# Performance work log

Hardware: AMD Instinct MI355X
Metric: run time of the kernel (lower is better)

Reference implementation:

```python
import jax, jax.numpy as jnp
import numpy as np
import math

TEMP = 30.0          # softmax temperature in RelationUnit
EPS_L2 = 1e-12       # F.normalize eps
EPS_IN = 1e-5        # InstanceL2Norm eps

def _l2n(x):
    n = jnp.sqrt(jnp.sum(x * x, axis=-1, keepdims=True))
    return x / jnp.maximum(n, EPS_L2)

def com_attn(qr, qi, kr, ki, vr, vi, Wk, bk):
    # seq layout [L, B, D]; complex QK^T with shared WK projection, per-branch softmax
    pr = _l2n(qr @ Wk + bk); pi = _l2n(qi @ Wk + bk)
    sr = _l2n(kr @ Wk + bk); si = _l2n(ki @ Wk + bk)
    dr = jnp.einsum('qbd,kbd->bqk', pr, sr) - jnp.einsum('qbd,kbd->bqk', pi, si)
    di = jnp.einsum('qbd,kbd->bqk', pr, si) + jnp.einsum('qbd,kbd->bqk', pi, sr)
    Ar = jax.nn.softmax(dr * TEMP, axis=-1)
    Ai = jax.nn.softmax(di * TEMP, axis=-1)
    outr = jnp.einsum('bqk,kbd->qbd', Ar, vr) - jnp.einsum('bqk,kbd->qbd', Ai, vi)
    outi = jnp.einsum('bqk,kbd->qbd', Ar, vi) + jnp.einsum('bqk,kbd->qbd', Ai, vr)
    return outr, outi

def inorm(src, n, b, d, h, w, scale):
    # src: [n*h*w, b, d] -> per-(img,batch) L2 instance norm over (d,h,w)
    x = src.reshape(n, h, w, b, d).transpose(0, 3, 4, 1, 2).reshape(n * b, d, h, w)
    cnt = float(d * h * w)
    ss = jnp.sum(x * x, axis=(1, 2, 3), keepdims=True)
    x = x * (scale * jnp.sqrt(cnt / (ss + EPS_IN)))
    return x.reshape(n, b, d, h * w).transpose(0, 3, 1, 2).reshape(n * h * w, b, d)

def to_seq(x):
    n, b, d, h, w = x.shape
    return x.reshape(n, b, d, h * w).transpose(0, 3, 1, 2).reshape(n * h * w, b, d)

def setup_inputs() -> dict:
    key = jax.random.key(0)
    ks = jax.random.split(key, 10)
    NT, NS, B, D, H, W, KD = 3, 3, 8, 512, 22, 22, 128
    f = jnp.float32
    return {
        'train_feat': jax.random.normal(ks[0], (NT, B, D, H, W), f),
        'test_feat': jax.random.normal(ks[1], (NS, B, D, H, W), f),
        'train_label': jax.random.uniform(ks[2], (NT, B, H, W), f),
        'Wk_en': jax.random.normal(ks[3], (D, D), f) * 0.02,
        'bk_en': jax.random.normal(ks[4], (D,), f) * 0.02,
        'Wk_self': jax.random.normal(ks[5], (D, KD), f) * 0.02,
        'bk_self': jax.random.normal(ks[6], (KD,), f) * 0.02,
        'Wk_cross': jax.random.normal(ks[7], (D, KD), f) * 0.02,
        'bk_cross': jax.random.normal(ks[8], (KD,), f) * 0.02,
        'Wc': jax.random.normal(ks[9], (D, 2 * D), f) * 0.02,
    }

def reference(train_feat, test_feat, train_label, Wk_en, bk_en, Wk_self, bk_self, Wk_cross, bk_cross, Wc):
    nt, b, d, h, w = train_feat.shape
    ns = test_feat.shape[0]
    scale = math.sqrt(1.0 / (d * 4 * 4))
    # ---- encoder (imag branch starts at zero) ----
    sr = to_seq(train_feat)
    si = jnp.zeros_like(sr)
    ar, ai = com_attn(sr, si, sr, si, sr, si, Wk_en, bk_en)
    mem_r = inorm(sr + ar, nt, b, d, h, w, scale)
    mem_i = inorm(si + ai, nt, b, d, h, w, scale)
    # ---- positional (label) map broadcast to feature dim ----
    pr = train_label.reshape(nt, b, 1, h * w).transpose(0, 3, 1, 2).reshape(nt * h * w, b, 1)
    pr = jnp.broadcast_to(pr, (nt * h * w, b, d))
    pi = jnp.zeros_like(pr)
    # ---- single decoder layer, applied per image (memory/pos shared) ----
    def dec(tr, ti):
        inl = lambda s: inorm(s, 1, b, d, h, w, scale)
        s2r, s2i = com_attn(tr, ti, tr, ti, tr, ti, Wk_self, bk_self)
        t1r = inl(tr + s2r); t1i = inl(ti + s2i)
        mkr, mki = com_attn(t1r, t1i, mem_r, mem_i, pr, pi, Wk_cross, bk_cross)
        t2r = inl(t1r * mkr); t2i = inl(t1i * mki)
        c3r, c3i = com_attn(t1r, t1i, mem_r, mem_i, mem_r * pr, mem_i * pi, Wk_cross, bk_cross)
        t4r = inl(t1r + c3r); t4i = inl(t1i + c3i)
        outr = inl(t2r + t4r); outi = inl(t2i + t4i)
        fr = outr.reshape(h, w, b, d).transpose(2, 3, 0, 1)  # [b,d,h,w]
        fi = outi.reshape(h, w, b, d).transpose(2, 3, 0, 1)
        return fr, fi
    def per_img_seq(x):  # [n,b,d,h,w] -> [n, h*w, b, d]
        n = x.shape[0]
        return x.reshape(n, b, d, h * w).transpose(0, 3, 1, 2)
    tr_seq = per_img_seq(train_feat)
    enc_r, enc_i = jax.vmap(dec)(tr_seq, jnp.zeros_like(tr_seq))  # [nt,b,d,h,w]
    te_seq = per_img_seq(test_feat)
    dec_r, dec_i = jax.vmap(dec)(te_seq, jnp.zeros_like(te_seq))  # [ns,b,d,h,w]
    # ---- 1x1 compress conv on cat([real, imag], channel) ----
    enc_feat = jnp.einsum('nbchw,oc->nbohw', jnp.concatenate([enc_r, enc_i], axis=2), Wc).reshape(nt * b, d, h, w)
    dec_feat = jnp.einsum('nbchw,oc->nbohw', jnp.concatenate([dec_r, dec_i], axis=2), Wc).reshape(ns * b, d, h, w)
    return jnp.concatenate([enc_feat, dec_feat], axis=0)
```

## Files before the change

kernel.cpp:

```cpp
#include <hip/hip_runtime.h>


namespace {

constexpr int kNI = 3;
constexpr int kB  = 8;
constexpr int kD  = 512;
constexpr int kKD = 128;
constexpr int kHW = 484;
constexpr int kL  = kNI * kHW;
constexpr int kLp = 1456;
constexpr int kHWp = 488;
constexpr float kTemp = 30.0f;
constexpr float kCnt  = 247808.0f;
constexpr float kScaleN = 0.011048543456039806f;
constexpr int kR = kHW * kB;
constexpr int kR6 = 6 * kR;

#define CDIV(a, b) (((a) + (b) - 1) / (b))

typedef float f32x4 __attribute__((ext_vector_type(4)));
typedef unsigned int u32x4 __attribute__((ext_vector_type(4)));
typedef unsigned short u16b;

__device__ __forceinline__ float wsum(float v) {
#pragma unroll
  for (int o = 32; o; o >>= 1) v += __shfl_down(v, o);
  return v;
}
__device__ __forceinline__ float wmax(float v) {
#pragma unroll
  for (int o = 32; o; o >>= 1) v = fmaxf(v, __shfl_down(v, o));
  return v;
}

__device__ __forceinline__ unsigned pk2bf(float lo, float hi) {
  union { float f; unsigned u; } a, b;
  a.f = lo; b.f = hi;
  unsigned ra = (a.u + 0x7FFFu + ((a.u >> 16) & 1u)) >> 16;
  unsigned rb = (b.u + 0x7FFFu + ((b.u >> 16) & 1u)) >> 16;
  return (ra & 0xFFFFu) | (rb << 16);
}
__device__ __forceinline__ u16b f2bf(float x) {
  union { float f; unsigned u; } a;
  a.f = x;
  return (u16b)((a.u + 0x7FFFu + ((a.u >> 16) & 1u)) >> 16);
}
__device__ __forceinline__ float bf2f(u16b x) {
  union { unsigned u; float f; } a;
  a.u = (unsigned)x << 16;
  return a.f;
}

__device__ __forceinline__ void mfma_bf16(f32x4& d, const u32x4& a, const u32x4& b) {
  asm("v_mfma_f32_16x16x32_bf16 %0, %1, %2, %0" : "+v"(d) : "v"(a), "v"(b));
}

__device__ __forceinline__ void ldsbar() {
  asm volatile("s_waitcnt lgkmcnt(0)" ::: "memory");
  __builtin_amdgcn_s_barrier();
  asm volatile("" ::: "memory");
}

__global__ void k_toseq(const float* __restrict__ in, float* __restrict__ out) {
  __shared__ float tile[32][33];
  int nb = blockIdx.z;
  int n = nb / kB, b = nb % kB;
  int p0 = blockIdx.x * 32, d0 = blockIdx.y * 32;
  int tx = threadIdx.x, ty = threadIdx.y;
#pragma unroll
  for (int j = 0; j < 4; ++j) {
    int d = d0 + ty + j * 8, p = p0 + tx;
    if (d < kD && p < kHW) tile[ty + j * 8][tx] = in[(long)nb * kD * kHW + (long)d * kHW + p];
  }
  __syncthreads();
#pragma unroll
  for (int j = 0; j < 4; ++j) {
    int p = p0 + ty + j * 8, d = d0 + tx;
    if (p < kHW && d < kD)
      out[((long)(n * kHW + p) * kB + b) * kD + d] = tile[tx][ty + j * 8];
  }
}

__global__ void k_cvt2d(const float* __restrict__ in, u16b* __restrict__ out, int C, int Cp) {
  long r = blockIdx.x;
  for (int c = threadIdx.x; c < C; c += 256)
    out[r * Cp + c] = f2bf(in[r * (long)C + c]);
}

__global__ void k_tcvt(const float* __restrict__ in, u16b* __restrict__ out, int R, int C) {
  __shared__ float tile[32][33];
  int c0 = blockIdx.x * 32, r0 = blockIdx.y * 32;
  int tx = threadIdx.x, ty = threadIdx.y;
#pragma unroll
  for (int j = 0; j < 4; ++j) {
    int r = r0 + ty + j * 8, c = c0 + tx;
    if (r < R && c < C) tile[ty + j * 8][tx] = in[(long)r * C + c];
  }
  __syncthreads();
#pragma unroll
  for (int j = 0; j < 4; ++j) {
    int c = c0 + ty + j * 8, r = r0 + tx;
    if (r < R && c < C) out[(long)c * R + r] = f2bf(tile[tx][ty + j * 8]);
  }
}

__global__ void k_vrt(const float* __restrict__ mr, const float* __restrict__ lab,
                      u16b* __restrict__ vt) {
  __shared__ float tile[32][33];
  int l0 = blockIdx.x * 32, d0 = blockIdx.y * 32, b = blockIdx.z;
  int tx = threadIdx.x, ty = threadIdx.y;
#pragma unroll
  for (int j = 0; j < 4; ++j) {
    int l = l0 + ty + j * 8;
    if (l < kL)
      tile[ty + j * 8][tx] = mr[((long)l * kB + b) * kD + d0 + tx] * lab[(long)l * kB + b];
  }
  __syncthreads();
#pragma unroll
  for (int j = 0; j < 4; ++j) {
    int d = d0 + ty + j * 8, l = l0 + tx;
    if (l < kL) vt[((long)b * kD + d) * kLp + l] = f2bf(tile[tx][ty + j * 8]);
  }
}

__global__ void k_lab(const float* __restrict__ tl, float* __restrict__ lab) {
  long i = (long)blockIdx.x * 256 + threadIdx.x;
  const long tot = (long)kNI * kB * kHW;
  if (i >= tot) return;
  int p = (int)(i % kHW);
  long t = i / kHW;
  int b = (int)(t % kB);
  int n = (int)(t / kB);
  lab[(long)(n * kHW + p) * kB + b] = tl[i];
}

__global__ void k_l2n_vec(const float* __restrict__ src, float* __restrict__ u, int C) {
  __shared__ float red[2];
  int tid = threadIdx.x;
  float s = 0.f;
  for (int c = tid; c < C; c += 128) { float x = src[c]; s += x * x; }
  s = wsum(s);
  if ((tid & 63) == 0) red[tid >> 6] = s;
  __syncthreads();
  float inv = 1.f / fmaxf(sqrtf(red[0] + red[1]), 1e-12f);
  for (int c = tid; c < C; c += 128) u[c] = src[c] * inv;
}

template <int BM, int BN, bool AF32, bool ACC>
__global__ __launch_bounds__(256) void k_gemm(const void* Ap, const u16b* __restrict__ B,
                                              float* __restrict__ C, int M, int N, int K,
                                              int lda, int ldb, int ldc,
                                              long sA1, long sA2, long sB1, long sB2,
                                              long sC1, long sC2,
                                              const float* __restrict__ addv) {
  const int gx = gridDim.x, gy = gridDim.y;
  const int nwg = gx * gy * gridDim.z;
  const int orig = (blockIdx.z * gy + blockIdx.y) * gx + blockIdx.x;
  const int q = nwg >> 3, rr = nwg & 7, xcd = orig & 7, idx = orig >> 3;
  const int swz = (xcd < rr ? xcd * (q + 1) : rr * (q + 1) + (xcd - rr) * q) + idx;
  const int bx = swz % gx;
  const int tmp = swz / gx;
  const int by = tmp % gy, bz = tmp / gy;
  const int za = bz >> 3, zb = bz & 7;

  const char* Ab = (const char*)Ap + (za * sA1 + zb * sA2) * (AF32 ? 4 : 2);
  const u16b* Bb = B + za * sB1 + zb * sB2;
  C += za * sC1 + zb * sC2;
  constexpr int FM = BM / 32, FN = BN / 32;
  constexpr int NSA = BM * 8 / 256;
  constexpr int NSB = BN * 8 / 256;
  const int m0 = by * BM, n0 = bx * BN;
  const int tid = threadIdx.x;
  const int wid = tid >> 6, lane = tid & 63;
  const int wr = wid >> 1, wc = wid & 1;
  const int fr = lane & 15, fk = lane >> 4;

  __shared__ unsigned AsU[BM * 36];
  __shared__ unsigned BsU[BN * 36];
  f32x4 acc[FM][FN] = {};

  u32x4 pa[NSA];
  float4 paf[AF32 ? 2 * NSA : 1];
  u32x4 pb[NSB];

  auto loadA = [&](int k0) {
#pragma unroll
    for (int i = 0; i < NSA; ++i) {
      int si = tid + i * 256;
      int row = si >> 3, c = si & 7;
      int gr = m0 + row, gk = k0 + c * 8;
      if constexpr (AF32) {
        const float* A = (const float*)Ab;
        if (gr < M && gk + 8 <= K) {
          const float* ap = A + (long)gr * lda + gk;
          paf[2 * i] = *(const float4*)ap;
          paf[2 * i + 1] = *(const float4*)(ap + 4);
        } else {
          float v[8];
#pragma unroll
          for (int j = 0; j < 8; ++j)
            v[j] = (gr < M && gk + j < K) ? A[(long)gr * lda + gk + j] : 0.f;
          paf[2 * i] = make_float4(v[0], v[1], v[2], v[3]);
          paf[2 * i + 1] = make_float4(v[4], v[5], v[6], v[7]);
        }
      } else {
        const u16b* A = (const u16b*)Ab;
        if (gr < M && gk + 8 <= K) {
          pa[i] = *(const u32x4*)(A + (long)gr * lda + gk);
        } else {
          unsigned v[8];
#pragma unroll
          for (int j = 0; j < 8; ++j)
            v[j] = (gr < M && gk + j < K) ? A[(long)gr * lda + gk + j] : 0u;
          pa[i].x = v[0] | (v[1] << 16); pa[i].y = v[2] | (v[3] << 16);
          pa[i].z = v[4] | (v[5] << 16); pa[i].w = v[6] | (v[7] << 16);
        }
      }
    }
  };
  auto loadB = [&](int k0) {
#pragma unroll
    for (int i = 0; i < NSB; ++i) {
      int si = tid + i * 256;
      int row = si >> 3, c = si & 7;
      int gr = n0 + row, gk = k0 + c * 8;
      if (gr < N && gk + 8 <= K) {
        pb[i] = *(const u32x4*)(Bb + (long)gr * ldb + gk);
      } else {
        unsigned v[8];
#pragma unroll
        for (int j = 0; j < 8; ++j)
          v[j] = (gr < N && gk + j < K) ? Bb[(long)gr * ldb + gk + j] : 0u;
        pb[i].x = v[0] | (v[1] << 16); pb[i].y = v[2] | (v[3] << 16);
        pb[i].z = v[4] | (v[5] << 16); pb[i].w = v[6] | (v[7] << 16);
      }
    }
  };
  auto storeAB = [&]() {
#pragma unroll
    for (int i = 0; i < NSA; ++i) {
      int si = tid + i * 256;
      int row = si >> 3, c = si & 7;
      u32x4 w;
      if constexpr (AF32) {
        float4 u0 = paf[2 * i], u1 = paf[2 * i + 1];
        w.x = pk2bf(u0.x, u0.y); w.y = pk2bf(u0.z, u0.w);
        w.z = pk2bf(u1.x, u1.y); w.w = pk2bf(u1.z, u1.w);
      } else {
        w = pa[i];
      }
      *(u32x4*)&AsU[row * 36 + c * 4] = w;
    }
#pragma unroll
    for (int i = 0; i < NSB; ++i) {
      int si = tid + i * 256;
      int row = si >> 3, c = si & 7;
      *(u32x4*)&BsU[row * 36 + c * 4] = pb[i];
    }
  };

  loadA(0);
  loadB(0);
  storeAB();
  __syncthreads();
  const int nk = CDIV(K, 64);
  for (int t = 0; t < nk; ++t) {
    const bool more = (t + 1 < nk);
    if (more) { loadA((t + 1) * 64); loadB((t + 1) * 64); }
#pragma unroll
    for (int kk = 0; kk < 2; ++kk) {
      u32x4 af[FM], bf[FN];
#pragma unroll
      for (int mi = 0; mi < FM; ++mi)
        af[mi] = *(const u32x4*)&AsU[(wr * (BM / 2) + mi * 16 + fr) * 36 + kk * 16 + fk * 4];
#pragma unroll
      for (int ni = 0; ni < FN; ++ni)
        bf[ni] = *(const u32x4*)&BsU[(wc * (BN / 2) + ni * 16 + fr) * 36 + kk * 16 + fk * 4];
#pragma unroll
      for (int mi = 0; mi < FM; ++mi)
#pragma unroll
        for (int ni = 0; ni < FN; ++ni) mfma_bf16(acc[mi][ni], af[mi], bf[ni]);
    }
    if (more) {
      __syncthreads();
      storeAB();
      __syncthreads();
    }
  }
  asm volatile("s_nop 7\n\ts_nop 7" ::: );
#pragma unroll
  for (int mi = 0; mi < FM; ++mi) {
#pragma unroll
    for (int r = 0; r < 4; ++r) {
      int gm = m0 + wr * (BM / 2) + mi * 16 + fk * 4 + r;
      if (gm >= M) continue;
      float av = addv ? addv[(long)za * (kD * 8) + (long)gm * 8 + zb] : 0.f;
#pragma unroll
      for (int ni = 0; ni < FN; ++ni) {
        int gn = n0 + wc * (BN / 2) + ni * 16 + fr;
        if (gn >= N) continue;
        long idx2 = (long)gm * ldc + gn;
        float v = acc[mi][ni][r] + av;
        C[idx2] = ACC ? (C[idx2] + v) : v;
      }
    }
  }
}

template <bool LAB, bool KIMG, bool VZ>
__global__ __launch_bounds__(256) void k_flash(const u16b* __restrict__ Q,
                                               const u16b* __restrict__ K,
                                               const u16b* __restrict__ V,
                                               const float* __restrict__ labv,
                                               u16b* __restrict__ O,
                                               float* __restrict__ mkout,
                                               int S, int ldv) {
  int orig = blockIdx.x;
  int b = orig & 7;
  int t = orig >> 3;
  int qt0 = (t & 15) * 32;
  int img = t >> 4;
  int z = img * 8 + b;
  int tid = threadIdx.x, wid = tid >> 6, lane = tid & 63;
  int fr = lane & 15, fk = lane >> 4;

  __shared__ float Ssm[32 * 68];
  __shared__ unsigned Plds[32 * 36];
  __shared__ float mrun[32], lrun[32], scal[32], mka[32];

  const long qbase = ((long)img * kR + b) * kKD;
  const long kbase = KIMG ? ((long)img * kR + b) * kKD : (long)b * kKD;
  const long vbase = (long)(VZ ? z : b) * kD * ldv;

  u32x4 afq[2][4];
#pragma unroll
  for (int mi = 0; mi < 2; ++mi) {
    int qq = qt0 + mi * 16 + fr;
    if (qq >= kHW) qq = kHW - 1;
#pragma unroll
    for (int kk = 0; kk < 4; ++kk)
      afq[mi][kk] = *(const u32x4*)(Q + qbase + (long)qq * (kB * kKD) + kk * 32 + fk * 8);
  }

  f32x4 oacc[2][8] = {};
  if (tid < 32) { mrun[tid] = -3.0e38f; lrun[tid] = 0.f; mka[tid] = 0.f; }
  __syncthreads();

  int r8 = lane >> 3, i8 = lane & 7;
  int srow = wid * 8 + r8;

  u32x4 kcur[4], knxt[4];
  {
    int krow = wid * 16 + fr;
    int kc = krow < S ? krow : S - 1;
    const u16b* kp = K + kbase + (long)kc * (kB * kKD);
#pragma unroll
    for (int kk = 0; kk < 4; ++kk) kcur[kk] = *(const u32x4*)(kp + kk * 32 + fk * 8);
  }

  for (int kt = 0; kt < S; kt += 64) {
    f32x4 sacc[2] = {};
#pragma unroll
    for (int kk = 0; kk < 4; ++kk) {
      mfma_bf16(sacc[0], afq[0][kk], kcur[kk]);
      mfma_bf16(sacc[1], afq[1][kk], kcur[kk]);
    }
    u32x4 vreg[2][8];
#pragma unroll
    for (int kk = 0; kk < 2; ++kk) {
      int kidx = kt + kk * 32 + fk * 8;
      if (kidx > ldv - 8) kidx = ldv - 8;
#pragma unroll
      for (int n = 0; n < 8; ++n) {
        int d = wid * 128 + n * 16 + fr;
        vreg[kk][n] = *(const u32x4*)(V + vbase + (long)d * ldv + kidx);
      }
    }
    const bool more = (kt + 64 < S);
    if (more) {
      int krow2 = kt + 64 + wid * 16 + fr;
      int kc2 = krow2 < S ? krow2 : S - 1;
      const u16b* kp2 = K + kbase + (long)kc2 * (kB * kKD);
#pragma unroll
      for (int kk = 0; kk < 4; ++kk) knxt[kk] = *(const u32x4*)(kp2 + kk * 32 + fk * 8);
    }
    asm volatile("s_nop 7\n\ts_nop 7" ::: );
    {
      int krow = kt + wid * 16 + fr;
      if (krow >= S) {
#pragma unroll
        for (int mi = 0; mi < 2; ++mi)
#pragma unroll
          for (int r = 0; r < 4; ++r) sacc[mi][r] = -1.0e30f;
      }
#pragma unroll
      for (int mi = 0; mi < 2; ++mi)
#pragma unroll
        for (int r = 0; r < 4; ++r)
          Ssm[(mi * 16 + fk * 4 + r) * 68 + wid * 16 + fr] = sacc[mi][r];
    }
    ldsbar();
    {
      float v[8];
      float mx = -3.0e38f;
#pragma unroll
      for (int j = 0; j < 8; ++j) {
        v[j] = Ssm[srow * 68 + i8 * 8 + j] * kTemp;
        mx = fmaxf(mx, v[j]);
      }
#pragma unroll
      for (int o = 1; o < 8; o <<= 1) mx = fmaxf(mx, __shfl_xor(mx, o));
      float mold = mrun[srow];
      float mnew = fmaxf(mold, mx);
      float p[8], ts = 0.f, lacc = 0.f;
#pragma unroll
      for (int j = 0; j < 8; ++j) {
        p[j] = __expf(v[j] - mnew);
        ts += p[j];
        if (LAB) {
          int kidx = kt + i8 * 8 + j;
          lacc += p[j] * labv[(long)(kidx < S ? kidx : S - 1) * kB + b];
        }
      }
#pragma unroll
      for (int o = 1; o < 8; o <<= 1) ts += __shfl_xor(ts, o);
      if (LAB) {
#pragma unroll
        for (int o = 1; o < 8; o <<= 1) lacc += __shfl_xor(lacc, o);
      }
      u32x4 w0;
      w0.x = pk2bf(p[0], p[1]); w0.y = pk2bf(p[2], p[3]);
      w0.z = pk2bf(p[4], p[5]); w0.w = pk2bf(p[6], p[7]);
      *(u32x4*)&Plds[srow * 36 + i8 * 4] = w0;
      if (i8 == 0) {
        float sc = __expf(mold - mnew);
        mrun[srow] = mnew;
        lrun[srow] = lrun[srow] * sc + ts;
        scal[srow] = sc;
        if (LAB) mka[srow] = mka[srow] * sc + lacc;
      }
    }
    ldsbar();
#pragma unroll
    for (int mi = 0; mi < 2; ++mi)
#pragma unroll
      for (int r = 0; r < 4; ++r) {
        float sc = scal[mi * 16 + fk * 4 + r];
#pragma unroll
        for (int n = 0; n < 8; ++n) oacc[mi][n][r] *= sc;
      }
    asm volatile("s_nop 7" ::: );
#pragma unroll
    for (int kk = 0; kk < 2; ++kk) {
      u32x4 ap0 = *(const u32x4*)&Plds[fr * 36 + kk * 16 + fk * 4];
      u32x4 ap1 = *(const u32x4*)&Plds[(16 + fr) * 36 + kk * 16 + fk * 4];
#pragma unroll
      for (int n = 0; n < 8; ++n) {
        mfma_bf16(oacc[0][n], ap0, vreg[kk][n]);
        mfma_bf16(oacc[1][n], ap1, vreg[kk][n]);
      }
    }
    asm volatile("s_nop 7\n\ts_nop 7" ::: );
    if (more) {
#pragma unroll
      for (int kk = 0; kk < 4; ++kk) kcur[kk] = knxt[kk];
    }
  }
  asm volatile("s_nop 7\n\ts_nop 7" ::: );
  __syncthreads();
#pragma unroll
  for (int mi = 0; mi < 2; ++mi)
#pragma unroll
    for (int r = 0; r < 4; ++r) {
      int qq = mi * 16 + fk * 4 + r;
      int gq = qt0 + qq;
      if (gq >= kHW) continue;
      float invl = 1.0f / lrun[qq];
      long orow = ((long)img * kR + (long)gq * kB + b) * kD;
#pragma unroll
      for (int n = 0; n < 8; ++n)
        O[orow + wid * 128 + n * 16 + fr] = f2bf(oacc[mi][n][r] * invl);
    }
  if (LAB && tid < 32) {
    int gq = qt0 + tid;
    if (gq < kHW) mkout[(long)img * kR + (long)gq * kB + b] = mka[tid] / lrun[tid];
  }
}

__global__ void k_bias_l2n(float* __restrict__ P, const float* __restrict__ bias, int C,
                           u16b* __restrict__ outb, const float* __restrict__ u,
                           float* __restrict__ g, int L) {
  __shared__ float red[2];
  long row = blockIdx.x;
  float* p = P + row * C;
  int tid = threadIdx.x;
  int nv = C >> 7;
  float v[4];
  float s = 0.f;
#pragma unroll
  for (int i = 0; i < 4; ++i)
    if (i < nv) {
      float x = p[tid + (i << 7)] + bias[tid + (i << 7)];
      v[i] = x;
      s += x * x;
    }
  s = wsum(s);
  if ((tid & 63) == 0) red[tid >> 6] = s;
  __syncthreads();
  float inv = 1.f / fmaxf(sqrtf(red[0] + red[1]), 1e-12f);
  float dot = 0.f;
#pragma unroll
  for (int i = 0; i < 4; ++i)
    if (i < nv) {
      float x = v[i] * inv;
      p[tid + (i << 7)] = x;
      outb[row * C + tid + (i << 7)] = f2bf(x);
      if (u) dot += x * u[tid + (i << 7)];
    }
  if (u) {
    __syncthreads();
    dot = wsum(dot);
    if ((tid & 63) == 0) red[tid >> 6] = dot;
    __syncthreads();
    if (tid == 0) {
      int img = (int)(row / kR);
      int within = (int)(row % kR);
      int qq = within >> 3, b = within & 7;
      g[((long)(img * 8 + b)) * L + qq] = red[0] + red[1];
    }
  }
}

__global__ __launch_bounds__(256) void k_softmax(float* __restrict__ S, int Lq, int Lk,
                                                 u16b* __restrict__ outb, int ldo) {
  __shared__ float sm[1456];
  __shared__ float red[4];
  int row = blockIdx.x;
  float* Sr = S + (long)row * Lk;
  int tid = threadIdx.x;
  float mx = -3.0e38f;
  for (int k = tid; k < Lk; k += 256) {
    float v = Sr[k] * kTemp;
    sm[k] = v;
    mx = fmaxf(mx, v);
  }
  mx = wmax(mx);
  if ((tid & 63) == 0) red[tid >> 6] = mx;
  __syncthreads();
  mx = fmaxf(fmaxf(red[0], red[1]), fmaxf(red[2], red[3]));
  __syncthreads();
  float s = 0.f;
  for (int k = tid; k < Lk; k += 256) {
    float e = __expf(sm[k] - mx);
    sm[k] = e;
    s += e;
  }
  s = wsum(s);
  if ((tid & 63) == 0) red[tid >> 6] = s;
  __syncthreads();
  float inv = 1.0f / (red[0] + red[1] + red[2] + red[3]);
  for (int k = tid; k < Lk; k += 256) {
    float p = sm[k] * inv;
    if (outb) outb[(long)row * ldo + k] = f2bf(p); else Sr[k] = p;
  }
}

__global__ __launch_bounds__(256) void k_cwi(const float* __restrict__ vb,
                                             const u16b* __restrict__ Krb,
                                             const float* __restrict__ labv,
                                             float* __restrict__ wI,
                                             float* __restrict__ mki8) {
  __shared__ float sm[kL];
  __shared__ float vbl[kKD];
  __shared__ float red[4];
  int z = blockIdx.x, b = z & 7;
  int tid = threadIdx.x;
  if (tid < kKD) vbl[tid] = vb[(long)z * kKD + tid];
  __syncthreads();
  float mx = -3.0e38f;
  for (int k = tid; k < kL; k += 256) {
    const u16b* kp = Krb + ((long)k * kB + b) * kKD;
    float s = 0.f;
    for (int c = 0; c < kKD; c += 8) {
      u32x4 w = *(const u32x4*)(kp + c);
      s += vbl[c] * bf2f((u16b)(w.x & 0xFFFF)) + vbl[c + 1] * bf2f((u16b)(w.x >> 16));
      s += vbl[c + 2] * bf2f((u16b)(w.y & 0xFFFF)) + vbl[c + 3] * bf2f((u16b)(w.y >> 16));
      s += vbl[c + 4] * bf2f((u16b)(w.z & 0xFFFF)) + vbl[c + 5] * bf2f((u16b)(w.z >> 16));
      s += vbl[c + 6] * bf2f((u16b)(w.w & 0xFFFF)) + vbl[c + 7] * bf2f((u16b)(w.w >> 16));
    }
    sm[k] = s * kTemp;
    mx = fmaxf(mx, sm[k]);
  }
  mx = wmax(mx);
  if ((tid & 63) == 0) red[tid >> 6] = mx;
  __syncthreads();
  mx = fmaxf(fmaxf(red[0], red[1]), fmaxf(red[2], red[3]));
  __syncthreads();
  float s = 0.f;
  for (int k = tid; k < kL; k += 256) {
    float e = __expf(sm[k] - mx);
    sm[k] = e;
    s += e;
  }
  s = wsum(s);
  if ((tid & 63) == 0) red[tid >> 6] = s;
  __syncthreads();
  float inv = 1.0f / (red[0] + red[1] + red[2] + red[3]);
  __syncthreads();
  float dot = 0.f;
  for (int k = tid; k < kL; k += 256) {
    float p = sm[k] * inv;
    wI[(long)z * kL + k] = p;
    dot += p * labv[(long)k * kB + b];
  }
  dot = wsum(dot);
  if ((tid & 63) == 0) red[tid >> 6] = dot;
  __syncthreads();
  if (tid == 0) mki8[z] = red[0] + red[1] + red[2] + red[3];
}

__global__ void k_wrowA(const float* __restrict__ g, const float* __restrict__ seq,
                        float* __restrict__ row2) {
  int z = blockIdx.y, img = z >> 3, b = z & 7;
  int c = blockIdx.z;
  int d = blockIdx.x * 128 + threadIdx.x;
  int k0 = c * 61;
  int k1 = min(kHW, k0 + 61);
  float s = 0.f;
  for (int k = k0; k < k1; ++k)
    s += g[(long)z * kHW + k] * seq[((long)img * kR + (long)k * kB + b) * kD + d];
  row2[((long)z * 8 + c) * kD + d] = s;
}

__global__ void k_wrowB(const float* __restrict__ row2, float* __restrict__ row) {
  int idx = blockIdx.x * 256 + threadIdx.x;
  int z = idx >> 9, d = idx & 511;
  float s = 0.f;
#pragma unroll
  for (int c = 0; c < 8; ++c) s += row2[((long)z * 8 + c) * kD + d];
  row[(long)z * kD + d] = s;
}

__global__ __launch_bounds__(256) void k_ss1f(const float* __restrict__ A,
                                              const float* __restrict__ B2,
                                              float* __restrict__ part) {
  __shared__ float red[4];
  long r = blockIdx.x;
  int tid = threadIdx.x;
  long base = r * kD;
  float z0 = A[base + tid] + B2[base + tid];
  float z1 = A[base + tid + 256] + B2[base + tid + 256];
  float s = z0 * z0 + z1 * z1;
  s = wsum(s);
  if ((tid & 63) == 0) red[tid >> 6] = s;
  __syncthreads();
  if (tid == 0) part[r] = red[0] + red[1] + red[2] + red[3];
}

__global__ __launch_bounds__(256) void k_scale1f(const float* __restrict__ A,
                                                 const float* __restrict__ B2,
                                                 float* __restrict__ outp,
                                                 const float* __restrict__ ss,
                                                 u16b* __restrict__ ob) {
  long r = blockIdx.x;
  int l = (int)(r / kB), b = (int)(r % kB);
  int g = (l / kHW) * kB + b;
  int tid = threadIdx.x;
  float fac = kScaleN * sqrtf(kCnt / (ss[g] + 1e-5f));
  long base = r * kD;
  float x0 = (A[base + tid] + B2[base + tid]) * fac;
  float x1 = (A[base + tid + 256] + B2[base + tid + 256]) * fac;
  outp[base + tid] = x0;
  outp[base + tid + 256] = x1;
  ob[base + tid] = f2bf(x0);
  ob[base + tid + 256] = f2bf(x1);
}

__global__ __launch_bounds__(256) void k_ss1b(const float* __restrict__ A,
                                              const u16b* __restrict__ B2,
                                              float* __restrict__ part) {
  __shared__ float red[4];
  long r = blockIdx.x;
  int tid = threadIdx.x;
  long base = r * kD;
  float z0 = A[base + tid] + bf2f(B2[base + tid]);
  float z1 = A[base + tid + 256] + bf2f(B2[base + tid + 256]);
  float s = z0 * z0 + z1 * z1;
  s = wsum(s);
  if ((tid & 63) == 0) red[tid >> 6] = s;
  __syncthreads();
  if (tid == 0) part[r] = red[0] + red[1] + red[2] + red[3];
}

__global__ void k_ssred(const float* __restrict__ part, float* __restrict__ ss, int R, int NG) {
  __shared__ float red[8];
  int g = blockIdx.x, v = blockIdx.y;
  int n = g / kB, b = g % kB;
  int tid = threadIdx.x;
  float s = 0.f;
  for (int p = tid; p < kHW; p += 512) s += part[(long)v * R + ((long)(n * kHW + p) * kB + b)];
  s = wsum(s);
  if ((tid & 63) == 0) red[tid >> 6] = s;
  __syncthreads();
  if (tid == 0) {
    float t = 0.f;
#pragma unroll
    for (int i = 0; i < 8; ++i) t += red[i];
    ss[(long)v * NG + g] = t;
  }
}

__global__ __launch_bounds__(256) void k_scale1b(const float* __restrict__ A,
                                                 const u16b* __restrict__ B2,
                                                 const float* __restrict__ ss,
                                                 u16b* __restrict__ ob) {
  long r = blockIdx.x;
  int img = (int)(r / kR), b = (int)(r & 7);
  int g = img * 8 + b;
  int tid = threadIdx.x;
  float fac = kScaleN * sqrtf(kCnt / (ss[g] + 1e-5f));
  long base = r * kD;
  ob[base + tid] = f2bf((A[base + tid] + bf2f(B2[base + tid])) * fac);
  ob[base + tid + 256] = f2bf((A[base + tid + 256] + bf2f(B2[base + tid + 256])) * fac);
}

__global__ void k_ti8(const float* __restrict__ row, float* __restrict__ ti8) {
  __shared__ float red[4];
  int z = blockIdx.x;
  int tid = threadIdx.x;
  float r0 = row[(long)z * kD + tid], r1 = row[(long)z * kD + tid + 256];
  float s = r0 * r0 + r1 * r1;
  s = wsum(s);
  if ((tid & 63) == 0) red[tid >> 6] = s;
  __syncthreads();
  float ssv = (float)kHW * (red[0] + red[1] + red[2] + red[3]);
  float fac = kScaleN * sqrtf(kCnt / (ssv + 1e-5f));
  ti8[(long)z * kD + tid] = r0 * fac;
  ti8[(long)z * kD + tid + 256] = r1 * fac;
}

__global__ void k_vb(const float* __restrict__ ti8, const float* __restrict__ Wk,
                     const float* __restrict__ bk, float* __restrict__ vb) {
  __shared__ float part[4][128];
  __shared__ float red[2];
  int z = blockIdx.x;
  int j = threadIdx.x;
  int dz = threadIdx.y;
  const float* row = ti8 + (long)z * kD;
  float acc = 0.f;
  int d0 = dz * 128;
  for (int d = d0; d < d0 + 128; ++d) acc += row[d] * Wk[(long)d * kKD + j];
  part[dz][j] = acc;
  __syncthreads();
  if (dz == 0) {
    float a = part[0][j] + part[1][j] + part[2][j] + part[3][j] + bk[j];
    float s = a * a;
    s = wsum(s);
    if ((j & 63) == 0) red[j >> 6] = s;
    part[0][j] = a;
  }
  __syncthreads();
  if (dz == 0) {
    float inv = 1.f / fmaxf(sqrtf(red[0] + red[1]), 1e-12f);
    vb[(long)z * kKD + j] = part[0][j] * inv;
  }
}

__global__ void k_ci8(const float* __restrict__ wI, const u16b* __restrict__ VrT,
                      float* __restrict__ ci8) {
  int idx = blockIdx.x * 4 + (threadIdx.x >> 6);
  int z = idx >> 9, d = idx & 511;
  int b = z & 7;
  int lane = threadIdx.x & 63;
  const float* w = wI + (long)z * kL;
  const u16b* vt = VrT + ((long)b * kD + d) * kLp;
  float s = 0.f;
  for (int l = lane; l < kL; l += 64) s += w[l] * bf2f(vt[l]);
  s = wsum(s);
  if (lane == 0) ci8[(long)z * kD + d] = s;
}

__global__ __launch_bounds__(256) void k_ss3b(const u16b* __restrict__ t1b,
                                              const float* __restrict__ mkr,
                                              const u16b* __restrict__ c3b,
                                              float* __restrict__ part) {
  __shared__ float red[4][3];
  long r = blockIdx.x;
  int tid = threadIdx.x;
  long base = r * kD;
  float mk = mkr[r];
  float s0 = 0.f, s1 = 0.f, s2 = 0.f;
#pragma unroll
  for (int j = 0; j < 2; ++j) {
    int d = tid + j * 256;
    float t = bf2f(t1b[base + d]);
    float a = t * mk;
    float bb = t + bf2f(c3b[base + d]);
    s0 += a * a; s1 += bb * bb; s2 += a * bb;
  }
  int w = tid >> 6, lane = tid & 63;
  float t0 = wsum(s0), t1 = wsum(s1), t2 = wsum(s2);
  if (lane == 0) { red[w][0] = t0; red[w][1] = t1; red[w][2] = t2; }
  __syncthreads();
  if (tid < 3)
    part[(long)tid * kR6 + r] = red[0][tid] + red[1][tid] + red[2][tid] + red[3][tid];
}

__global__ __launch_bounds__(512) void k_coef(const float* __restrict__ ssp,
                                              const float* __restrict__ ti8,
                                              const float* __restrict__ ci8,
                                              const float* __restrict__ mki8,
                                              float* __restrict__ coef,
                                              float* __restrict__ oi8) {
  __shared__ float cai[8], cbi[8];
  int img = blockIdx.x;
  int tid = threadIdx.x;
  int b = tid >> 6, lane = tid & 63;
  int z = img * 8 + b;
  float sT = 0.f, sU = 0.f, sV = 0.f;
  for (int d = lane; d < kD; d += 64) {
    float ti = ti8[(long)z * kD + d], ci = ci8[(long)z * kD + d];
    float u = ti + ci;
    sT += ti * ti; sU += u * u; sV += ti * u;
  }
  sT = wsum(sT); sU = wsum(sU); sV = wsum(sV);
  if (lane == 0) {
    float SSa = ssp[z], SSb = ssp[48 + z], SSab = ssp[96 + z];
    float f2 = kScaleN * sqrtf(kCnt / (SSa + 1e-5f));
    float f4 = kScaleN * sqrtf(kCnt / (SSb + 1e-5f));
    float ssz = f2 * f2 * SSa + f4 * f4 * SSb + 2.f * f2 * f4 * SSab;
    float fac = kScaleN * sqrtf(kCnt / (ssz + 1e-5f));
    coef[img * 16 + b] = f2 * fac;
    coef[img * 16 + 8 + b] = f4 * fac;
    float mk = mki8[z];
    float SSai = (float)kHW * mk * mk * sT;
    float SSbi = (float)kHW * sU;
    float SSabi = (float)kHW * mk * sV;
    float f2i = kScaleN * sqrtf(kCnt / (SSai + 1e-5f));
    float f4i = kScaleN * sqrtf(kCnt / (SSbi + 1e-5f));
    float sszi = f2i * f2i * SSai + f4i * f4i * SSbi + 2.f * f2i * f4i * SSabi;
    float faci = kScaleN * sqrtf(kCnt / (sszi + 1e-5f));
    cai[b] = f2i * faci;
    cbi[b] = f4i * faci;
  }
  __syncthreads();
#pragma unroll
  for (int j = 0; j < 8; ++j) {
    int i = tid * 8 + j;
    int bb = i >> 9, d = i & 511;
    int zz = img * 8 + bb;
    float ti = ti8[(long)zz * kD + d], ci = ci8[(long)zz * kD + d];
    oi8[(long)img * 4096 + i] = ti * mki8[zz] * cai[bb] + (ti + ci) * cbi[bb];
  }
}

__global__ void k_oadd(const float* __restrict__ Wc, const float* __restrict__ oi8,
                       float* __restrict__ oadd) {
  int idx = blockIdx.x * 4 + (threadIdx.x >> 6);
  int img = idx >> 12, rem = idx & 4095;
  int o = rem >> 3, b = rem & 7;
  int lane = threadIdx.x & 63;
  const float* wrow = Wc + (long)o * 1024 + 512;
  const float* oi = oi8 + (long)img * 4096 + (long)b * kD;
  float s = 0.f;
  for (int d = lane; d < kD; d += 64) s += wrow[d] * oi[d];
  s = wsum(s);
  if (lane == 0) oadd[(long)img * 4096 + o * 8 + b] = s;
}

__global__ __launch_bounds__(256) void k_zfinb(const u16b* __restrict__ t1b,
                                               const float* __restrict__ mkr,
                                               const u16b* __restrict__ c3b,
                                               const float* __restrict__ coef,
                                               u16b* __restrict__ t2b) {
  long r = blockIdx.x;
  int img = (int)(r / kR), b = (int)(r & 7);
  int tid = threadIdx.x;
  float mk = mkr[r];
  float ca = coef[img * 16 + b], cb = coef[img * 16 + 8 + b];
  long base = r * kD;
#pragma unroll
  for (int j = 0; j < 2; ++j) {
    int d = tid + j * 256;
    float t = bf2f(t1b[base + d]);
    float ov = t * mk * ca + (t + bf2f(c3b[base + d])) * cb;
    t2b[base + d] = f2bf(ov);
  }
}

template <int BM, int BN, bool AF32, bool ACC>
void gemm(hipStream_t s, const void* A, const u16b* B, float* C, int M, int N, int K, int lda,
          int ldb, int ldc, long sA1, long sA2, long sB1, long sB2, long sC1, long sC2,
          int batch, const float* addv = nullptr) {
  dim3 grd(CDIV(N, BN), CDIV(M, BM), batch), blk(256);
  k_gemm<BM, BN, AF32, ACC><<<grd, blk, 0, s>>>(A, B, C, M, N, K, lda, ldb, ldc, sA1, sA2,
                                                sB1, sB2, sC1, sC2, addv);
}

}

extern "C" void kernel_launch(void* const* d_in, const int* in_sizes, int n_in, void* d_out,
                              int out_size, void* d_ws, size_t ws_size, hipStream_t stream) {
  (void)in_sizes; (void)n_in; (void)out_size;
  const float* tf  = (const float*)d_in[0];
  const float* sf  = (const float*)d_in[1];
  const float* tl  = (const float*)d_in[2];
  const float* WkE = (const float*)d_in[3];
  const float* bkE = (const float*)d_in[4];
  const float* WkS = (const float*)d_in[5];
  const float* bkS = (const float*)d_in[6];
  const float* WkC = (const float*)d_in[7];
  const float* bkC = (const float*)d_in[8];
  const float* Wc  = (const float*)d_in[9];
  float* out = (float*)d_out;
  float* ws = (float*)d_ws;

  const long LBD = (long)kL * kB * kD;
  const long LBK = (long)kL * kB * kKD;

  long off = 0;
  auto alloc = [&](long n) { long o = off; off += (n + 255) & ~255L; return o; };
  auto allocU = [&](long nu) { return alloc((nu + 1) / 2); };

  long o_seqT = alloc(LBD);
  long o_seqS = alloc(LBD);
  long o_Kr   = alloc(LBK);
  long o_Krb  = allocU(LBK);
  long o_VrT  = allocU((long)kB * kD * kLp);
  long o_tfb  = allocU((long)kNI * kB * kD * kHWp);
  long o_sfb  = allocU((long)kNI * kB * kD * kHWp);
  long o_WkTE = allocU((long)kD * kD);
  long o_WkTS = allocU((long)kKD * kD);
  long o_WkTC = allocU((long)kKD * kD);
  long o_Wcb  = allocU((long)kD * 2 * kD);
  long o_lab  = alloc((long)kL * kB);
  long o_uS   = alloc(kKD);
  long o_vb   = alloc(48L * kKD);
  long o_g    = alloc(48L * kHW);
  long o_wI   = alloc(48L * kL);
  long o_row  = alloc(48L * kD);
  long o_row2 = alloc(48L * 8 * kD);
  long o_mkr  = alloc((long)kR6);
  long o_mki8 = alloc(48);
  long o_ti8  = alloc(48L * kD);
  long o_ci8  = alloc(48L * kD);
  long o_oi8  = alloc(48L * kD);
  long o_oadd = alloc(6L * kD * 8);
  long o_ss   = alloc(512);
  long o_part = alloc(3L * kR6);
  long o_scr  = off;

  long o_Pe  = o_scr;
  long o_Peb = o_Pe + LBD;
  long o_Ae  = o_Peb + LBD / 2;
  long o_Aeb = o_Ae + (long)kB * kL * kL;
  long enc_end = o_Aeb + (8L * kL * kLp + 1) / 2;
  long o_ar  = o_Pe;
  long o_mr  = o_Ae;

  long p = o_scr;
  auto nxt = [&](long n) { long o = p; p += (n + 255) & ~255L; return o; };
  long o_Ps   = nxt((long)kR6 * kKD);
  long o_Psb  = nxt(((long)kR6 * kKD + 1) / 2);
  long o_Pcb  = nxt(((long)kR6 * kKD + 1) / 2);
  long o_s2rb = nxt(((long)kR6 * kD + 1) / 2);
  long o_t1rb = nxt(((long)kR6 * kD + 1) / 2);
  long o_c3rb = nxt(((long)kR6 * kD + 1) / 2);
  long o_t2b  = nxt(((long)kR6 * kD + 1) / 2);
  long img_end = p;

  long total = (enc_end > img_end ? enc_end : img_end);
  if ((size_t)total * sizeof(float) > ws_size) return;

  float* seqT = ws + o_seqT;
  float* Kr = ws + o_Kr;
  u16b* Krb = (u16b*)(ws + o_Krb);
  u16b* VrT = (u16b*)(ws + o_VrT);
  u16b* tfb = (u16b*)(ws + o_tfb);
  float* lab = ws + o_lab;
  float* uS = ws + o_uS;
  float* vb = ws + o_vb;
  float* g_ = ws + o_g;
  float* wI = ws + o_wI;
  float* row = ws + o_row;
  float* row2 = ws + o_row2;
  float* mkr = ws + o_mkr;
  float* mki8 = ws + o_mki8;
  float* ti8 = ws + o_ti8;
  float* ci8 = ws + o_ci8;
  float* oi8 = ws + o_oi8;
  float* oadd = ws + o_oadd;
  float* ssp = ws + o_ss;
  float* coef = ssp + 160;
  float* part = ws + o_part;
  float* Pe = ws + o_Pe;
  u16b* Peb = (u16b*)(ws + o_Peb);
  float* Ae = ws + o_Ae;
  u16b* Aeb = (u16b*)(ws + o_Aeb);
  float* ar = ws + o_ar;
  float* mr = ws + o_mr;
  u16b* mrb = (u16b*)(ws + o_mr + LBD);
  float* Ps = ws + o_Ps;
  u16b* Psb = (u16b*)(ws + o_Psb);
  u16b* Pcb = (u16b*)(ws + o_Pcb);
  u16b* s2rb = (u16b*)(ws + o_s2rb);
  u16b* t1rb = (u16b*)(ws + o_t1rb);
  u16b* c3rb = (u16b*)(ws + o_c3rb);
  u16b* t2b = (u16b*)(ws + o_t2b);
  u16b* WkTE = (u16b*)(ws + o_WkTE);
  u16b* WkTS = (u16b*)(ws + o_WkTS);
  u16b* WkTC = (u16b*)(ws + o_WkTC);
  u16b* Wcb = (u16b*)(ws + o_Wcb);

  {
    dim3 grd(CDIV(kHW, 32), CDIV(kD, 32), kNI * kB), blk(32, 8);
    k_toseq<<<grd, blk, 0, stream>>>(tf, seqT);
    k_toseq<<<grd, blk, 0, stream>>>(sf, ws + o_seqS);
  }
  k_cvt2d<<<kNI * kB * kD, 256, 0, stream>>>(tf, tfb, kHW, kHWp);
  k_cvt2d<<<kNI * kB * kD, 256, 0, stream>>>(sf, (u16b*)(ws + o_sfb), kHW, kHWp);
  k_cvt2d<<<kD, 256, 0, stream>>>(Wc, Wcb, 2 * kD, 2 * kD);
  k_tcvt<<<dim3(kD / 32, kD / 32), dim3(32, 8), 0, stream>>>(WkE, WkTE, kD, kD);
  k_tcvt<<<dim3(kKD / 32, kD / 32), dim3(32, 8), 0, stream>>>(WkS, WkTS, kD, kKD);
  k_tcvt<<<dim3(kKD / 32, kD / 32), dim3(32, 8), 0, stream>>>(WkC, WkTC, kD, kKD);
  k_lab<<<CDIV(kNI * kB * kHW, 256), 256, 0, stream>>>(tl, lab);
  k_l2n_vec<<<1, 128, 0, stream>>>(bkS, uS, kKD);

  gemm<64, 128, true, false>(stream, seqT, WkTE, Pe, kL * kB, kD, kD, kD, kD, kD,
                             0, 0, 0, 0, 0, 0, 1);
  k_bias_l2n<<<kL * kB, 128, 0, stream>>>(Pe, bkE, kD, Peb, nullptr, nullptr, 0);
  gemm<128, 128, false, false>(stream, Peb, Peb, Ae, kL, kL, kD, kB * kD, kB * kD, kL,
                               0, kD, 0, kD, 0, (long)kL * kL, 8);
  k_softmax<<<kB * kL, 256, 0, stream>>>(Ae, kL, kL, Aeb, kLp);
  gemm<64, 128, false, false>(stream, Aeb, tfb, ar, kL, kD, kHW, kLp, kHWp, kB * kD,
                              0, (long)kL * kLp, 0, (long)kD * kHWp, 0, kD, 8);
  gemm<64, 128, false, true>(stream, Aeb + kHW, tfb + (long)kB * kD * kHWp, ar, kL, kD, kHW,
                             kLp, kHWp, kB * kD, 0, (long)kL * kLp, 0, (long)kD * kHWp, 0, kD,
                             8);
  gemm<64, 128, false, true>(stream, Aeb + 2 * kHW, tfb + 2L * kB * kD * kHWp, ar, kL, kD,
                             kHW, kLp, kHWp, kB * kD, 0, (long)kL * kLp, 0, (long)kD * kHWp,
                             0, kD, 8);
  k_ss1f<<<kL * kB, 256, 0, stream>>>(seqT, ar, part);
  k_ssred<<<dim3(kNI * kB, 1), 512, 0, stream>>>(part, ssp, kL * kB, kNI * kB);
  k_scale1f<<<kL * kB, 256, 0, stream>>>(seqT, ar, mr, ssp, mrb);
  k_vrt<<<dim3(CDIV(kL, 32), kD / 32, kB), dim3(32, 8), 0, stream>>>(mr, lab, VrT);
  gemm<64, 64, false, false>(stream, mrb, WkTC, Kr, kL * kB, kKD, kD, kD, kD, kKD,
                             0, 0, 0, 0, 0, 0, 1);
  k_bias_l2n<<<kL * kB, 128, 0, stream>>>(Kr, bkC, kKD, Krb, nullptr, nullptr, 0);

  gemm<64, 128, true, false>(stream, seqT, WkTS, Ps, kR6, kKD, kD, kD, kD, kKD,
                             0, 0, 0, 0, 0, 0, 1);
  k_bias_l2n<<<kR6, 128, 0, stream>>>(Ps, bkS, kKD, Psb, uS, g_, kHW);
  k_softmax<<<48, 256, 0, stream>>>(g_, 1, kHW, nullptr, 0);
  k_wrowA<<<dim3(kD / 128, 48, 8), 128, 0, stream>>>(g_, seqT, row2);
  k_wrowB<<<48 * kD / 256, 256, 0, stream>>>(row2, row);
  k_ti8<<<48, 256, 0, stream>>>(row, ti8);
  k_vb<<<48, dim3(128, 4), 0, stream>>>(ti8, WkC, bkC, vb);
  k_flash<false, true, true><<<768, 256, 0, stream>>>(Psb, Psb, tfb, nullptr, s2rb,
                                                      nullptr, kHW, kHWp);
  k_ss1b<<<kR6, 256, 0, stream>>>(seqT, s2rb, part);
  k_ssred<<<dim3(48, 1), 512, 0, stream>>>(part, ssp, kR6, 48);
  k_scale1b<<<kR6, 256, 0, stream>>>(seqT, s2rb, ssp, t1rb);
  gemm<64, 128, false, false>(stream, t1rb, WkTC, Ps, kR6, kKD, kD, kD, kD, kKD,
                              0, 0, 0, 0, 0, 0, 1);
  k_bias_l2n<<<kR6, 128, 0, stream>>>(Ps, bkC, kKD, Pcb, nullptr, nullptr, 0);
  k_cwi<<<48, 256, 0, stream>>>(vb, Krb, lab, wI, mki8);
  k_ci8<<<48 * 512 / 4, 256, 0, stream>>>(wI, VrT, ci8);
  k_flash<true, false, false><<<768, 256, 0, stream>>>(Pcb, Krb, VrT, lab, c3rb,
                                                       mkr, kL, kLp);
  k_ss3b<<<kR6, 256, 0, stream>>>(t1rb, mkr, c3rb, part);
  k_ssred<<<dim3(48, 3), 512, 0, stream>>>(part, ssp, kR6, 48);
  k_coef<<<6, 512, 0, stream>>>(ssp, ti8, ci8, mki8, coef, oi8);
  k_oadd<<<6 * 4096 / 4, 256, 0, stream>>>(Wc, oi8, oadd);
  k_zfinb<<<kR6, 256, 0, stream>>>(t1rb, mkr, c3rb, coef, t2b);
  gemm<64, 64, false, false>(stream, Wcb, t2b, out, kD, kHW, kD, 2 * kD, kB * kD, kHW,
                             0, 0, (long)kR * kD, kD, 8L * kD * kHW, (long)kD * kHW, 48, oadd);
}
```

Before: 810.0 us.

## Repack flash-attention V into 8-column chunk-major layout and raise MFMA priority

```diff
diff --git a/kernel.cpp b/kernel.cpp
--- a/kernel.cpp
+++ b/kernel.cpp
@@ -16,6 +16,8 @@
 constexpr float kScaleN = 0.011048543456039806f;
 constexpr int kR = kHW * kB;
 constexpr int kR6 = 6 * kR;
+constexpr int kP8s = kHWp / 8;
+constexpr int kP8c = kLp / 8;
 
 #define CDIV(a, b) (((a) + (b) - 1) / (b))
 
@@ -122,6 +124,19 @@
     int d = d0 + ty + j * 8, l = l0 + tx;
     if (l < kL) vt[((long)b * kD + d) * kLp + l] = f2bf(tile[tx][ty + j * 8]);
   }
+}
+
+__global__ void k_vpack(const u16b* __restrict__ in, u16b* __restrict__ out,
+                        int ldv, int P, int Sreal) {
+  long idx = (long)blockIdx.x * 256 + threadIdx.x;
+  int j = (int)(idx & 7);
+  int d = (int)((idx >> 3) & 511);
+  long t = idx >> 12;
+  int c8 = (int)(t % P);
+  int z = (int)(t / P);
+  int col = c8 * 8 + j;
+  u16b v = (col < Sreal) ? in[((long)z * kD + d) * ldv + col] : (u16b)0;
+  out[idx] = v;
 }
 
 __global__ void k_lab(const float* __restrict__ tl, float* __restrict__ lab) {
@@ -311,11 +326,11 @@
 template <bool LAB, bool KIMG, bool VZ>
 __global__ __launch_bounds__(256) void k_flash(const u16b* __restrict__ Q,
                                                const u16b* __restrict__ K,
-                                               const u16b* __restrict__ V,
+                                               const u16b* __restrict__ V8,
                                                const float* __restrict__ labv,
                                                u16b* __restrict__ O,
                                                float* __restrict__ mkout,
-                                               int S, int ldv) {
+                                               int S, int P8) {
   int orig = blockIdx.x;
   int b = orig & 7;
   int t = orig >> 3;
@@ -331,7 +346,7 @@
 
   const long qbase = ((long)img * kR + b) * kKD;
   const long kbase = KIMG ? ((long)img * kR + b) * kKD : (long)b * kKD;
-  const long vbase = (long)(VZ ? z : b) * kD * ldv;
+  const long vbase = (long)(VZ ? z : b) * P8 * kD * 8;
 
   u32x4 afq[2][4];
 #pragma unroll
@@ -361,20 +376,23 @@
 
   for (int kt = 0; kt < S; kt += 64) {
     f32x4 sacc[2] = {};
+    __builtin_amdgcn_s_setprio(1);
 #pragma unroll
     for (int kk = 0; kk < 4; ++kk) {
       mfma_bf16(sacc[0], afq[0][kk], kcur[kk]);
       mfma_bf16(sacc[1], afq[1][kk], kcur[kk]);
     }
+    __builtin_amdgcn_s_setprio(0);
     u32x4 vreg[2][8];
 #pragma unroll
     for (int kk = 0; kk < 2; ++kk) {
-      int kidx = kt + kk * 32 + fk * 8;
-      if (kidx > ldv - 8) kidx = ldv - 8;
+      int c8 = (kt >> 3) + kk * 4 + fk;
+      if (c8 > P8 - 1) c8 = P8 - 1;
+      const u16b* vp = V8 + vbase + (long)c8 * kD * 8;
 #pragma unroll
       for (int n = 0; n < 8; ++n) {
         int d = wid * 128 + n * 16 + fr;
-        vreg[kk][n] = *(const u32x4*)(V + vbase + (long)d * ldv + kidx);
+        vreg[kk][n] = *(const u32x4*)(vp + (long)d * 8);
       }
     }
     const bool more = (kt + 64 < S);
@@ -451,6 +469,7 @@
         for (int n = 0; n < 8; ++n) oacc[mi][n][r] *= sc;
       }
     asm volatile("s_nop 7" ::: );
+    __builtin_amdgcn_s_setprio(1);
 #pragma unroll
     for (int kk = 0; kk < 2; ++kk) {
       u32x4 ap0 = *(const u32x4*)&Plds[fr * 36 + kk * 16 + fk * 4];
@@ -461,6 +480,7 @@
         mfma_bf16(oacc[1][n], ap1, vreg[kk][n]);
       }
     }
+    __builtin_amdgcn_s_setprio(0);
     asm volatile("s_nop 7\n\ts_nop 7" ::: );
     if (more) {
 #pragma unroll
@@ -968,6 +988,8 @@
   long o_t1rb = nxt(((long)kR6 * kD + 1) / 2);
   long o_c3rb = nxt(((long)kR6 * kD + 1) / 2);
   long o_t2b  = nxt(((long)kR6 * kD + 1) / 2);
+  long o_V8s  = nxt((48L * kP8s * kD * 8 + 1) / 2);
+  long o_V8c  = nxt((8L * kP8c * kD * 8 + 1) / 2);
   long img_end = p;
 
   long total = (enc_end > img_end ? enc_end : img_end);
@@ -1008,6 +1030,8 @@
   u16b* t1rb = (u16b*)(ws + o_t1rb);
   u16b* c3rb = (u16b*)(ws + o_c3rb);
   u16b* t2b = (u16b*)(ws + o_t2b);
+  u16b* V8s = (u16b*)(ws + o_V8s);
+  u16b* V8c = (u16b*)(ws + o_V8c);
   u16b* WkTE = (u16b*)(ws + o_WkTE);
   u16b* WkTS = (u16b*)(ws + o_WkTS);
   u16b* WkTC = (u16b*)(ws + o_WkTC);
@@ -1049,6 +1073,8 @@
                              0, 0, 0, 0, 0, 0, 1);
   k_bias_l2n<<<kL * kB, 128, 0, stream>>>(Kr, bkC, kKD, Krb, nullptr, nullptr, 0);
 
+  k_vpack<<<48 * kP8s * kD * 8 / 256, 256, 0, stream>>>(tfb, V8s, kHWp, kP8s, kHW);
+  k_vpack<<<8 * kP8c * kD * 8 / 256, 256, 0, stream>>>(VrT, V8c, kLp, kP8c, kL);
   gemm<64, 128, true, false>(stream, seqT, WkTS, Ps, kR6, kKD, kD, kD, kD, kKD,
                              0, 0, 0, 0, 0, 0, 1);
   k_bias_l2n<<<kR6, 128, 0, stream>>>(Ps, bkS, kKD, Psb, uS, g_, kHW);
@@ -1057,8 +1083,8 @@
   k_wrowB<<<48 * kD / 256, 256, 0, stream>>>(row2, row);
   k_ti8<<<48, 256, 0, stream>>>(row, ti8);
   k_vb<<<48, dim3(128, 4), 0, stream>>>(ti8, WkC, bkC, vb);
-  k_flash<false, true, true><<<768, 256, 0, stream>>>(Psb, Psb, tfb, nullptr, s2rb,
-                                                      nullptr, kHW, kHWp);
+  k_flash<false, true, true><<<768, 256, 0, stream>>>(Psb, Psb, V8s, nullptr, s2rb,
+                                                      nullptr, kHW, kP8s);
   k_ss1b<<<kR6, 256, 0, stream>>>(seqT, s2rb, part);
   k_ssred<<<dim3(48, 1), 512, 0, stream>>>(part, ssp, kR6, 48);
   k_scale1b<<<kR6, 256, 0, stream>>>(seqT, s2rb, ssp, t1rb);
@@ -1067,8 +1093,8 @@
   k_bias_l2n<<<kR6, 128, 0, stream>>>(Ps, bkC, kKD, Pcb, nullptr, nullptr, 0);
   k_cwi<<<48, 256, 0, stream>>>(vb, Krb, lab, wI, mki8);
   k_ci8<<<48 * 512 / 4, 256, 0, stream>>>(wI, VrT, ci8);
-  k_flash<true, false, false><<<768, 256, 0, stream>>>(Pcb, Krb, VrT, lab, c3rb,
-                                                       mkr, kL, kLp);
+  k_flash<true, false, false><<<768, 256, 0, stream>>>(Pcb, Krb, V8c, lab, c3rb,
+                                                       mkr, kL, kP8c);
   k_ss3b<<<kR6, 256, 0, stream>>>(t1rb, mkr, c3rb, part);
   k_ssred<<<dim3(48, 3), 512, 0, stream>>>(part, ssp, kR6, 48);
   k_coef<<<6, 512, 0, stream>>>(ssp, ti8, ci8, mki8, coef, oi8);
```

Result: faster. 771.7 us (-4.7%).
